# Optimization experiments

Hardware: AMD Instinct MI355X
Metric: run time of the kernel (lower is better)

The kernel has to match this reference:

```python
import jax, jax.numpy as jnp
import numpy as np


def setup_inputs() -> dict:
    key = jax.random.key(0)
    k1, k2, k3, k4 = jax.random.split(key, 4)
    B, S, D = 4, 2048, 1024
    return {
        "x": jax.random.normal(k1, (B, S, D), dtype=jnp.float32),
        "wq": jax.random.normal(k2, (D, D), dtype=jnp.float32),
        "wk": jax.random.normal(k3, (D, D), dtype=jnp.float32),
        "wv": jax.random.normal(k4, (D, D), dtype=jnp.float32),
    }


def reference(x, wq, wk, wv):
    # q,k,v: [B,S,D]
    q = x @ wq
    k = x @ wk
    v = x @ wv
    # NOTE: source applies NO 1/sqrt(d) scaling; we match it faithfully.
    scores = jnp.einsum("bsd,btd->bst", q, k)  # [B,S,S]
    weights = jax.nn.softmax(scores, axis=-1)
    return jnp.einsum("bst,btd->bsd", weights, v)  # [B,S,D]
```

## Files before the change

kernel.cpp:

```cpp
#include <hip/hip_runtime.h>


typedef _Float16 half4_t __attribute__((ext_vector_type(4)));
typedef _Float16 half8_t __attribute__((ext_vector_type(8)));
typedef float f32x4 __attribute__((ext_vector_type(4)));

#define BM 128
#define BN 128
#define BK 32

__device__ __forceinline__ void gl_lds16(const _Float16* g, _Float16* l) {
    __builtin_amdgcn_global_load_lds(
        (const __attribute__((address_space(1))) unsigned int*)g,
        (__attribute__((address_space(3))) unsigned int*)l, 16, 0, 0);
}


__global__ __launch_bounds__(256) void conv_x_kernel(
    const float* __restrict__ in, _Float16* __restrict__ hi,
    _Float16* __restrict__ lo, int n4)
{
    int i = blockIdx.x * 256 + threadIdx.x;
    if (i >= n4) return;
    float4 v = ((const float4*)in)[i];
    float xs[4] = {v.x, v.y, v.z, v.w};
    half4_t h, l;
#pragma unroll
    for (int j = 0; j < 4; ++j) {
        _Float16 hh = (_Float16)xs[j];
        h[j] = hh;
        l[j] = (_Float16)(xs[j] - (float)hh);
    }
    ((half4_t*)hi)[i] = h;
    ((half4_t*)lo)[i] = l;
}

__global__ __launch_bounds__(256) void conv_w_kernel(
    const float* __restrict__ wq, const float* __restrict__ wk,
    const float* __restrict__ wv, _Float16* qh, _Float16* ql,
    _Float16* kh, _Float16* kl, _Float16* vh)
{
    __shared__ float tle[64][65];
    const int z = blockIdx.z;
    const float* w = (z == 0) ? wq : (z == 1) ? wk : wv;
    _Float16* oh = (z == 0) ? qh : (z == 1) ? kh : vh;
    _Float16* ol = (z == 0) ? ql : (z == 1) ? kl : nullptr;
    const int tr = blockIdx.y * 64, tc = blockIdx.x * 64;
    const int t16 = threadIdx.x & 15, tq = threadIdx.x >> 4;
#pragma unroll
    for (int j = 0; j < 4; ++j) {
        int lr = tq + j * 16;
        float4 v = *(const float4*)(w + (size_t)(tr + lr) * 1024 + tc + t16 * 4);
        tle[lr][t16 * 4 + 0] = v.x;
        tle[lr][t16 * 4 + 1] = v.y;
        tle[lr][t16 * 4 + 2] = v.z;
        tle[lr][t16 * 4 + 3] = v.w;
    }
    __syncthreads();
#pragma unroll
    for (int j = 0; j < 4; ++j) {
        int orow = tq + j * 16;
        int oc = t16 * 4;
        half4_t h, l;
#pragma unroll
        for (int i = 0; i < 4; ++i) {
            float xv = tle[oc + i][orow];
            _Float16 hh = (_Float16)xv;
            h[i] = hh;
            l[i] = (_Float16)(xv - (float)hh);
        }
        *(half4_t*)(oh + (size_t)(tc + orow) * 1024 + tr + oc) = h;
        if (ol) *(half4_t*)(ol + (size_t)(tc + orow) * 1024 + tr + oc) = l;
    }
}

template <bool OUTF32>
__global__ __launch_bounds__(256) void gemm_split(
    const _Float16* __restrict__ Ah, const _Float16* __restrict__ Al, size_t az,
    const _Float16* __restrict__ Bh, const _Float16* __restrict__ Bl, size_t bz,
    float* __restrict__ Cf, size_t cz, int ldc,
    _Float16* __restrict__ Oh, _Float16* __restrict__ Ol, size_t oz, int ldo,
    int lda, int ldb, int K)
{
    __shared__ __align__(16) _Float16 sAh[BM][BK], sAl[BM][BK];
    __shared__ __align__(16) _Float16 sBh[BN][BK], sBl[BN][BK];

    const int tid = threadIdx.x;
    const int wave = tid >> 6, lane = tid & 63;
    const int wm = (wave >> 1) * 64, wn = (wave & 1) * 64;
    const int lrow = lane & 15, quad = lane >> 4;
    const int bm = blockIdx.y * BM, bn = blockIdx.x * BN;
    const int z = blockIdx.z;

    const _Float16* pAh = Ah + (size_t)z * az;
    const _Float16* pAl = Al + (size_t)z * az;
    const _Float16* pBh = Bh + (size_t)z * bz;
    const _Float16* pBl = Bl + (size_t)z * bz;

    const int r0 = wave * 32 + (lane >> 2);
    const int kofs = (lane & 3) * 8;
    const size_t a0o = (size_t)(bm + r0) * lda + kofs;
    const size_t a1o = a0o + (size_t)16 * lda;
    const size_t b0o = (size_t)(bn + r0) * ldb + kofs;
    const size_t b1o = b0o + (size_t)16 * ldb;
    _Float16* lA0 = &sAh[r0][kofs];
    _Float16* lA1 = &sAh[r0 + 16][kofs];
    _Float16* lAl0 = &sAl[r0][kofs];
    _Float16* lAl1 = &sAl[r0 + 16][kofs];
    _Float16* lB0 = &sBh[r0][kofs];
    _Float16* lB1 = &sBh[r0 + 16][kofs];
    _Float16* lBl0 = &sBl[r0][kofs];
    _Float16* lBl1 = &sBl[r0 + 16][kofs];

    f32x4 acc[4][4];
#pragma unroll
    for (int i = 0; i < 4; ++i)
#pragma unroll
        for (int j = 0; j < 4; ++j) acc[i][j] = 0.0f;

    for (int k0 = 0; k0 < K; k0 += BK) {
        gl_lds16(pAh + a0o + k0, lA0);
        gl_lds16(pAh + a1o + k0, lA1);
        gl_lds16(pAl + a0o + k0, lAl0);
        gl_lds16(pAl + a1o + k0, lAl1);
        gl_lds16(pBh + b0o + k0, lB0);
        gl_lds16(pBh + b1o + k0, lB1);
        gl_lds16(pBl + b0o + k0, lBl0);
        gl_lds16(pBl + b1o + k0, lBl1);
        __syncthreads();

        half8_t a0[4], a1[4], b0[4], b1[4];
#pragma unroll
        for (int mt = 0; mt < 4; ++mt) {
            a0[mt] = *(const half8_t*)&sAh[wm + mt * 16 + lrow][quad * 8];
            a1[mt] = *(const half8_t*)&sAl[wm + mt * 16 + lrow][quad * 8];
        }
#pragma unroll
        for (int nt = 0; nt < 4; ++nt) {
            b0[nt] = *(const half8_t*)&sBh[wn + nt * 16 + lrow][quad * 8];
            b1[nt] = *(const half8_t*)&sBl[wn + nt * 16 + lrow][quad * 8];
        }
#pragma unroll
        for (int mt = 0; mt < 4; ++mt)
#pragma unroll
            for (int nt = 0; nt < 4; ++nt) {
                acc[mt][nt] = __builtin_amdgcn_mfma_f32_16x16x32_f16(a0[mt], b0[nt], acc[mt][nt], 0, 0, 0);
                acc[mt][nt] = __builtin_amdgcn_mfma_f32_16x16x32_f16(a0[mt], b1[nt], acc[mt][nt], 0, 0, 0);
                acc[mt][nt] = __builtin_amdgcn_mfma_f32_16x16x32_f16(a1[mt], b0[nt], acc[mt][nt], 0, 0, 0);
            }
        __syncthreads();
    }

#pragma unroll
    for (int mt = 0; mt < 4; ++mt)
#pragma unroll
        for (int nt = 0; nt < 4; ++nt)
#pragma unroll
            for (int r = 0; r < 4; ++r) {
                int gm = bm + wm + mt * 16 + quad * 4 + r;
                int gn = bn + wn + nt * 16 + lrow;
                float v = acc[mt][nt][r];
                if (OUTF32) {
                    Cf[(size_t)z * cz + (size_t)gm * ldc + gn] = v;
                } else {
                    _Float16 h = (_Float16)v;
                    Oh[(size_t)z * oz + (size_t)gm * ldo + gn] = h;
                    Ol[(size_t)z * oz + (size_t)gm * ldo + gn] = (_Float16)(v - (float)h);
                }
            }
}

template <bool TRANSOUT>
__global__ __launch_bounds__(256) void gemm_plain(
    const _Float16* __restrict__ Ag, size_t az,
    const _Float16* __restrict__ Bg, size_t bz,
    float* __restrict__ Cf, size_t cz, int ldc,
    _Float16* __restrict__ Ot,
    int lda, int ldb, int K)
{
    __shared__ __align__(16) _Float16 sA[BM][BK], sB[BN][BK];

    const int tid = threadIdx.x;
    const int wave = tid >> 6, lane = tid & 63;
    const int wm = (wave >> 1) * 64, wn = (wave & 1) * 64;
    const int lrow = lane & 15, quad = lane >> 4;
    const int bm = blockIdx.y * BM, bn = blockIdx.x * BN;
    const int z = blockIdx.z;

    const _Float16* pA = Ag + (size_t)z * az;
    const _Float16* pB = Bg + (size_t)z * bz;

    const int r0 = wave * 32 + (lane >> 2);
    const int kofs = (lane & 3) * 8;
    const size_t a0o = (size_t)(bm + r0) * lda + kofs;
    const size_t a1o = a0o + (size_t)16 * lda;
    const size_t b0o = (size_t)(bn + r0) * ldb + kofs;
    const size_t b1o = b0o + (size_t)16 * ldb;
    _Float16* lA0 = &sA[r0][kofs];
    _Float16* lA1 = &sA[r0 + 16][kofs];
    _Float16* lB0 = &sB[r0][kofs];
    _Float16* lB1 = &sB[r0 + 16][kofs];

    f32x4 acc[4][4];
#pragma unroll
    for (int i = 0; i < 4; ++i)
#pragma unroll
        for (int j = 0; j < 4; ++j) acc[i][j] = 0.0f;

    for (int k0 = 0; k0 < K; k0 += BK) {
        gl_lds16(pA + a0o + k0, lA0);
        gl_lds16(pA + a1o + k0, lA1);
        gl_lds16(pB + b0o + k0, lB0);
        gl_lds16(pB + b1o + k0, lB1);
        __syncthreads();

        half8_t a0[4], b0[4];
#pragma unroll
        for (int mt = 0; mt < 4; ++mt)
            a0[mt] = *(const half8_t*)&sA[wm + mt * 16 + lrow][quad * 8];
#pragma unroll
        for (int nt = 0; nt < 4; ++nt)
            b0[nt] = *(const half8_t*)&sB[wn + nt * 16 + lrow][quad * 8];
#pragma unroll
        for (int mt = 0; mt < 4; ++mt)
#pragma unroll
            for (int nt = 0; nt < 4; ++nt)
                acc[mt][nt] = __builtin_amdgcn_mfma_f32_16x16x32_f16(a0[mt], b0[nt], acc[mt][nt], 0, 0, 0);
        __syncthreads();
    }

#pragma unroll
    for (int mt = 0; mt < 4; ++mt)
#pragma unroll
        for (int nt = 0; nt < 4; ++nt) {
            int gm0 = bm + wm + mt * 16 + quad * 4;
            int gn = bn + wn + nt * 16 + lrow;
            if (TRANSOUT) {
                half4_t o;
#pragma unroll
                for (int r = 0; r < 4; ++r) o[r] = (_Float16)acc[mt][nt][r];
                *(half4_t*)(Ot + ((size_t)(gm0 >> 11) << 21) +
                            (size_t)gn * 2048 + (gm0 & 2047)) = o;
            } else {
#pragma unroll
                for (int r = 0; r < 4; ++r)
                    Cf[(size_t)z * cz + (size_t)(gm0 + r) * ldc + gn] = acc[mt][nt][r];
            }
        }
}

__global__ __launch_bounds__(256) void softmax_kernel(float* __restrict__ S)
{
    float* row = S + (size_t)blockIdx.x * 2048;
    float4* r4 = (float4*)row;
    const int tid = threadIdx.x;
    const int wave = tid >> 6, lane = tid & 63;

    float4 a = r4[tid], b = r4[tid + 256];
    float m = fmaxf(fmaxf(fmaxf(a.x, a.y), fmaxf(a.z, a.w)),
                    fmaxf(fmaxf(b.x, b.y), fmaxf(b.z, b.w)));
#pragma unroll
    for (int o = 32; o; o >>= 1) m = fmaxf(m, __shfl_xor(m, o));
    __shared__ float redm[4];
    __shared__ float reds[4];
    if (lane == 0) redm[wave] = m;
    __syncthreads();
    m = fmaxf(fmaxf(redm[0], redm[1]), fmaxf(redm[2], redm[3]));

    a.x = __expf(a.x - m); a.y = __expf(a.y - m);
    a.z = __expf(a.z - m); a.w = __expf(a.w - m);
    b.x = __expf(b.x - m); b.y = __expf(b.y - m);
    b.z = __expf(b.z - m); b.w = __expf(b.w - m);

    float s = a.x + a.y + a.z + a.w + b.x + b.y + b.z + b.w;
#pragma unroll
    for (int o = 32; o; o >>= 1) s += __shfl_xor(s, o);
    if (lane == 0) reds[wave] = s;
    __syncthreads();
    s = reds[0] + reds[1] + reds[2] + reds[3];

    float inv = 1.0f / s;
    _Float16* o16 = (_Float16*)row;
    half4_t ha, hb;
    ha[0] = (_Float16)(a.x * inv); ha[1] = (_Float16)(a.y * inv);
    ha[2] = (_Float16)(a.z * inv); ha[3] = (_Float16)(a.w * inv);
    hb[0] = (_Float16)(b.x * inv); hb[1] = (_Float16)(b.y * inv);
    hb[2] = (_Float16)(b.z * inv); hb[3] = (_Float16)(b.w * inv);
    ((half4_t*)o16)[tid] = ha;
    ((half4_t*)o16)[tid + 256] = hb;
}

extern "C" void kernel_launch(void* const* d_in, const int* in_sizes, int n_in,
                              void* d_out, int out_size, void* d_ws, size_t ws_size,
                              hipStream_t stream)
{
    const float* x  = (const float*)d_in[0];
    const float* wq = (const float*)d_in[1];
    const float* wk = (const float*)d_in[2];
    const float* wv = (const float*)d_in[3];
    float* out = (float*)d_out;

    const int S = 2048, D = 1024;
    const size_t M8 = 8ull << 20;
    const size_t M1 = 1ull << 20;
    char* ws = (char*)d_ws;

    _Float16* qh  = (_Float16*)(ws);
    _Float16* kh  = (_Float16*)(ws + (16ull << 20));
    _Float16* ql  = (_Float16*)(ws + (32ull << 20));
    _Float16* kl  = (_Float16*)(ws + (48ull << 20));
    _Float16* vT  = (_Float16*)(ws + (64ull << 20));
    _Float16* xh  = (_Float16*)(ws + (80ull << 20));
    _Float16* xl  = (_Float16*)(ws + (96ull << 20));
    _Float16* wqh = (_Float16*)(ws + (112ull << 20));
    _Float16* wkh = (_Float16*)(ws + (114ull << 20));
    _Float16* wql = (_Float16*)(ws + (116ull << 20));
    _Float16* wkl = (_Float16*)(ws + (118ull << 20));
    _Float16* wvh = (_Float16*)(ws + (120ull << 20));
    float*    sc  = (float*)(ws + (80ull << 20));

    dim3 blk(256);

    conv_x_kernel<<<dim3((int)(M8 / 4 / 256)), blk, 0, stream>>>(x, xh, xl, (int)(M8 / 4));
    conv_w_kernel<<<dim3(16, 16, 3), blk, 0, stream>>>(wq, wk, wv, wqh, wql, wkh, wkl, wvh);

    gemm_split<false><<<dim3(D / BN, 8192 / BM, 2), blk, 0, stream>>>(
        xh, xl, 0, wqh, wql, M1, nullptr, 0, 0, qh, ql, M8, D, D, D, D);

    gemm_plain<true><<<dim3(D / BN, 8192 / BM, 1), blk, 0, stream>>>(
        xh, 0, wvh, 0, nullptr, 0, 0, vT, D, D, D);

    gemm_split<true><<<dim3(S / BN, S / BM, 4), blk, 0, stream>>>(
        qh, ql, (size_t)S * D, kh, kl, (size_t)S * D, sc, (size_t)S * S, S,
        nullptr, nullptr, 0, 0, D, D, D);

    softmax_kernel<<<dim3(4 * S), blk, 0, stream>>>(sc);

    gemm_plain<false><<<dim3(D / BN, S / BM, 4), blk, 0, stream>>>(
        (const _Float16*)sc, (size_t)S * 4096, vT, (size_t)D * S,
        out, (size_t)S * D, D, nullptr, 4096, S, S);
}
```

Baseline: 435.9 us.

## Fold Wq·Wkᵀ into one matrix so scores use x·M·xᵀ

Reassociates the score computation as (x·(Wq·Wkᵀ))·xᵀ. A small 1024³ split-precision GEMM forms M = Wq·Wkᵀ, then a single projection y = x·M replaces the separate Q and K projections. The score GEMM then uses x directly in place of K, which removes one full 8192×1024×1024 projection GEMM. The weight conversion is restructured to match: Wq and Wk are split without transposing and Wv gets its own transpose kernel. The cost is a different floating-point rounding path, since M is rounded to a hi/lo fp16 pair, and with unscaled scores of large magnitude that can shift the softmax noticeably.

Result: no change. 431.9 us (-0.9%).

```diff
diff --git a/kernel.cpp b/kernel.cpp
--- a/kernel.cpp
+++ b/kernel.cpp
@@ -16,7 +16,7 @@
 }
 
 
-__global__ __launch_bounds__(256) void conv_x_kernel(
+__global__ __launch_bounds__(256) void conv_split_kernel(
     const float* __restrict__ in, _Float16* __restrict__ hi,
     _Float16* __restrict__ lo, int n4)
 {
@@ -35,16 +35,10 @@
     ((half4_t*)lo)[i] = l;
 }
 
-__global__ __launch_bounds__(256) void conv_w_kernel(
-    const float* __restrict__ wq, const float* __restrict__ wk,
-    const float* __restrict__ wv, _Float16* qh, _Float16* ql,
-    _Float16* kh, _Float16* kl, _Float16* vh)
+__global__ __launch_bounds__(256) void conv_wvT_kernel(
+    const float* __restrict__ w, _Float16* __restrict__ oh)
 {
     __shared__ float tle[64][65];
-    const int z = blockIdx.z;
-    const float* w = (z == 0) ? wq : (z == 1) ? wk : wv;
-    _Float16* oh = (z == 0) ? qh : (z == 1) ? kh : vh;
-    _Float16* ol = (z == 0) ? ql : (z == 1) ? kl : nullptr;
     const int tr = blockIdx.y * 64, tc = blockIdx.x * 64;
     const int t16 = threadIdx.x & 15, tq = threadIdx.x >> 4;
 #pragma unroll
@@ -61,16 +55,10 @@
     for (int j = 0; j < 4; ++j) {
         int orow = tq + j * 16;
         int oc = t16 * 4;
-        half4_t h, l;
-#pragma unroll
-        for (int i = 0; i < 4; ++i) {
-            float xv = tle[oc + i][orow];
-            _Float16 hh = (_Float16)xv;
-            h[i] = hh;
-            l[i] = (_Float16)(xv - (float)hh);
-        }
+        half4_t h;
+#pragma unroll
+        for (int i = 0; i < 4; ++i) h[i] = (_Float16)tle[oc + i][orow];
         *(half4_t*)(oh + (size_t)(tc + orow) * 1024 + tr + oc) = h;
-        if (ol) *(half4_t*)(ol + (size_t)(tc + orow) * 1024 + tr + oc) = l;
     }
 }
 
@@ -305,33 +293,38 @@
     const size_t M1 = 1ull << 20;
     char* ws = (char*)d_ws;
 
-    _Float16* qh  = (_Float16*)(ws);
-    _Float16* kh  = (_Float16*)(ws + (16ull << 20));
-    _Float16* ql  = (_Float16*)(ws + (32ull << 20));
-    _Float16* kl  = (_Float16*)(ws + (48ull << 20));
-    _Float16* vT  = (_Float16*)(ws + (64ull << 20));
-    _Float16* xh  = (_Float16*)(ws + (80ull << 20));
-    _Float16* xl  = (_Float16*)(ws + (96ull << 20));
-    _Float16* wqh = (_Float16*)(ws + (112ull << 20));
-    _Float16* wkh = (_Float16*)(ws + (114ull << 20));
-    _Float16* wql = (_Float16*)(ws + (116ull << 20));
-    _Float16* wkl = (_Float16*)(ws + (118ull << 20));
-    _Float16* wvh = (_Float16*)(ws + (120ull << 20));
-    float*    sc  = (float*)(ws + (80ull << 20));
+    _Float16* xh   = (_Float16*)(ws);
+    _Float16* xl   = (_Float16*)(ws + (16ull << 20));
+    _Float16* yh   = (_Float16*)(ws + (32ull << 20));
+    _Float16* yl   = (_Float16*)(ws + (48ull << 20));
+    _Float16* vT   = (_Float16*)(ws + (64ull << 20));
+    _Float16* wqh  = (_Float16*)(ws + (80ull << 20));
+    _Float16* wql  = (_Float16*)(ws + (82ull << 20));
+    _Float16* wkh  = (_Float16*)(ws + (84ull << 20));
+    _Float16* wkl  = (_Float16*)(ws + (86ull << 20));
+    _Float16* wvTh = (_Float16*)(ws + (88ull << 20));
+    _Float16* Mh   = (_Float16*)(ws + (90ull << 20));
+    _Float16* Ml   = (_Float16*)(ws + (92ull << 20));
+    float*    sc   = (float*)(ws + (94ull << 20));
 
     dim3 blk(256);
 
-    conv_x_kernel<<<dim3((int)(M8 / 4 / 256)), blk, 0, stream>>>(x, xh, xl, (int)(M8 / 4));
-    conv_w_kernel<<<dim3(16, 16, 3), blk, 0, stream>>>(wq, wk, wv, wqh, wql, wkh, wkl, wvh);
-
-    gemm_split<false><<<dim3(D / BN, 8192 / BM, 2), blk, 0, stream>>>(
-        xh, xl, 0, wqh, wql, M1, nullptr, 0, 0, qh, ql, M8, D, D, D, D);
+    conv_split_kernel<<<dim3((int)(M8 / 4 / 256)), blk, 0, stream>>>(x, xh, xl, (int)(M8 / 4));
+    conv_split_kernel<<<dim3((int)(M1 / 4 / 256)), blk, 0, stream>>>(wq, wqh, wql, (int)(M1 / 4));
+    conv_split_kernel<<<dim3((int)(M1 / 4 / 256)), blk, 0, stream>>>(wk, wkh, wkl, (int)(M1 / 4));
+    conv_wvT_kernel<<<dim3(16, 16), blk, 0, stream>>>(wv, wvTh);
+
+    gemm_split<false><<<dim3(8, 8, 1), blk, 0, stream>>>(
+        wkh, wkl, 0, wqh, wql, 0, nullptr, 0, 0, Mh, Ml, 0, D, D, D, D);
+
+    gemm_split<false><<<dim3(D / BN, 8192 / BM, 1), blk, 0, stream>>>(
+        xh, xl, 0, Mh, Ml, 0, nullptr, 0, 0, yh, yl, 0, D, D, D, D);
 
     gemm_plain<true><<<dim3(D / BN, 8192 / BM, 1), blk, 0, stream>>>(
-        xh, 0, wvh, 0, nullptr, 0, 0, vT, D, D, D);
+        xh, 0, wvTh, 0, nullptr, 0, 0, vT, D, D, D);
 
     gemm_split<true><<<dim3(S / BN, S / BM, 4), blk, 0, stream>>>(
-        qh, ql, (size_t)S * D, kh, kl, (size_t)S * D, sc, (size_t)S * S, S,
+        yh, yl, (size_t)S * D, xh, xl, (size_t)S * D, sc, (size_t)S * S, S,
         nullptr, nullptr, 0, 0, D, D, D);
 
     softmax_kernel<<<dim3(4 * S), blk, 0, stream>>>(sc);
```
